# Kernel tuning notes

Hardware: AMD Instinct MI355X
Metric: run time of the kernel (lower is better)

## Reference

```python
import jax, jax.numpy as jnp
import numpy as np

B, N, E, D, DE, H = 2, 50000, 300000, 128, 128, 128
LN_EPS = 1e-5


def setup_inputs() -> dict:
    key = jax.random.key(0)
    ks = jax.random.split(key, 8)
    return {
        "node_features": jax.random.normal(ks[0], (B, N, D), dtype=jnp.float32),
        "edge_features": jax.random.normal(ks[1], (B, E, DE), dtype=jnp.float32),
        "receivers": jax.random.randint(ks[2], (B, E), 0, N, dtype=jnp.int32),
        "W1": jax.random.normal(ks[3], (D + DE, H), dtype=jnp.float32) * (1.0 / np.sqrt(D + DE)),
        "b1": jnp.zeros((H,), dtype=jnp.float32),
        "W2": jax.random.normal(ks[4], (H, D), dtype=jnp.float32) * (1.0 / np.sqrt(H)),
        "b2": jnp.zeros((D,), dtype=jnp.float32),
        "ln_scale": jnp.ones((D,), dtype=jnp.float32),
        "ln_bias": jnp.zeros((D,), dtype=jnp.float32),
    }


def _scatter_mean(edge_features, receivers, n_nodes):
    # batched segment-mean: offset receivers per batch element, one flat segment_sum
    b, e, de = edge_features.shape
    seg = (receivers + jnp.arange(b, dtype=receivers.dtype)[:, None] * n_nodes).reshape(-1)
    sums = jax.ops.segment_sum(edge_features.reshape(b * e, de), seg, num_segments=b * n_nodes)
    cnt = jax.ops.segment_sum(jnp.ones((b * e,), edge_features.dtype), seg, num_segments=b * n_nodes)
    mean = sums / jnp.maximum(cnt, 1.0)[:, None]
    return mean.reshape(b, n_nodes, de)


def reference(node_features, edge_features, receivers, W1, b1, W2, b2, ln_scale, ln_bias):
    n = node_features.shape[1]
    agg = _scatter_mean(edge_features, receivers, n)          # [B, N, DE]
    feat = jnp.concatenate([node_features, agg], axis=-1)     # [B, N, D+DE]
    h = jax.nn.relu(feat @ W1 + b1)                           # [B, N, H]
    out = h @ W2 + b2                                         # [B, N, D]
    mu = jnp.mean(out, axis=-1, keepdims=True)
    var = jnp.mean(jnp.square(out - mu), axis=-1, keepdims=True)
    out = (out - mu) * jax.lax.rsqrt(var + LN_EPS) * ln_scale + ln_bias
    return node_features + out
```

## Files before the change

kernel.cpp:

```cpp
#include <hip/hip_runtime.h>
#include <hip/hip_bf16.h>

#define B_   2
#define N_   50000
#define E_   300000
#define D_   128
#define H_   128
#define K1_  256
#define MTOT (B_ * N_)
#define BM   64
#define CAP  32

typedef __bf16         bf16x8 __attribute__((ext_vector_type(8)));
typedef float          f32x4  __attribute__((ext_vector_type(4)));
typedef unsigned short u16x8  __attribute__((ext_vector_type(8)));
typedef unsigned short u16x4  __attribute__((ext_vector_type(4)));

__device__ __forceinline__ unsigned short f2bf(float f) {
    unsigned u = __builtin_bit_cast(unsigned, f);
    unsigned r = u + 0x7fffu + ((u >> 16) & 1u);
    return (unsigned short)(r >> 16);
}
__device__ __forceinline__ float bf2f(unsigned short h) {
    unsigned u = (unsigned)h << 16;
    return __builtin_bit_cast(float, u);
}

__global__ void wconv_kernel(const float* __restrict__ W1, const float* __restrict__ W2,
                             unsigned short* __restrict__ w1t, unsigned short* __restrict__ w2t,
                             int* __restrict__ deg) {
    int i = blockIdx.x * 256 + threadIdx.x;
    if (i < K1_ * H_) {
        int k = i / H_, n = i % H_;
        w1t[n * K1_ + k] = f2bf(W1[i]);
    }
    if (i < H_ * D_) {
        int k = i / D_, n = i % D_;
        w2t[n * H_ + k] = f2bf(W2[i]);
    }
    for (int j = i; j < MTOT; j += (K1_ * H_)) deg[j] = 0;
}

__global__ __launch_bounds__(256) void fill_kernel(const int* __restrict__ recv,
                                                   int* __restrict__ deg,
                                                   int* __restrict__ eidx) {
    int e = blockIdx.x * 256 + threadIdx.x;
    if (e >= B_ * E_) return;
    int b = e / E_;
    long t = (long)b * N_ + recv[e];
    int slot = atomicAdd(&deg[t], 1);
    if (slot < CAP) eidx[(long)slot * MTOT + t] = e;
}

#define SWZ(byte, row) ((byte) ^ (((row) & 7) << 4))

__global__ __launch_bounds__(256, 4) void fused_kernel(
        const float* __restrict__ nodef, const float* __restrict__ ef,
        const int* __restrict__ deg, const int* __restrict__ eidx,
        const unsigned short* __restrict__ w1t, const unsigned short* __restrict__ w2t,
        const float* __restrict__ b1, const float* __restrict__ b2,
        const float* __restrict__ lnsc, const float* __restrict__ lnbi,
        float* __restrict__ out) {
    __shared__ __align__(16) unsigned short sF[BM * K1_];
    char* sFb = (char*)sF;

    const int tid   = threadIdx.x;
    const long row0 = (long)blockIdx.x * BM;
    const int lane  = tid & 63;
    const int wave  = tid >> 6;

    const int nl = lane >> 2;
    const int ql = lane & 3;
    const int gr = wave * 16 + nl;
    const long ggrow = row0 + gr;
    int dg = 0;
    if (ggrow < MTOT) dg = deg[ggrow];
    int dgc = min(dg, CAP);
    int e0 = (dgc > 0) ? eidx[ggrow] : 0;

    {
        const int seg = tid & 15;
        const int rb  = tid >> 4;
        #pragma unroll
        for (int it = 0; it < 4; ++it) {
            int r = it * 16 + rb;
            long grow = row0 + r;
            u16x8 o;
            if (grow < MTOT) {
                const f32x4* p = (const f32x4*)&nodef[grow * 128 + seg * 8];
                f32x4 x = __builtin_nontemporal_load(p);
                f32x4 y = __builtin_nontemporal_load(p + 1);
                o[0] = f2bf(x[0]); o[1] = f2bf(x[1]);
                o[2] = f2bf(x[2]); o[3] = f2bf(x[3]);
                o[4] = f2bf(y[0]); o[5] = f2bf(y[1]);
                o[6] = f2bf(y[2]); o[7] = f2bf(y[3]);
            } else {
                #pragma unroll
                for (int q = 0; q < 8; ++q) o[q] = 0;
            }
            *(u16x8*)(sFb + SWZ(r * 512 + seg * 16, r)) = o;
        }
    }

    f32x4 ga[8];
    #pragma unroll
    for (int c = 0; c < 8; ++c) { f32x4 z = {0.f, 0.f, 0.f, 0.f}; ga[c] = z; }
    int e = e0;
    for (int i = 0; i < dgc; ++i) {
        int e_next = (i + 1 < dgc) ? eidx[(long)(i + 1) * MTOT + ggrow] : 0;
        const char* base = (const char*)ef + (long)e * 512 + ql * 16;
        #pragma unroll
        for (int c = 0; c < 8; ++c) {
            f32x4 v = __builtin_nontemporal_load((const f32x4*)(base + c * 64));
            ga[c] += v;
        }
        e = e_next;
    }
    {
        float inv = 1.0f / fmaxf((float)dg, 1.0f);
        #pragma unroll
        for (int c = 0; c < 8; ++c) {
            u16x4 o;
            o[0] = f2bf(ga[c][0] * inv); o[1] = f2bf(ga[c][1] * inv);
            o[2] = f2bf(ga[c][2] * inv); o[3] = f2bf(ga[c][3] * inv);
            *(u16x4*)(sFb + SWZ(gr * 512 + 256 + (c * 4 + ql) * 8, gr)) = o;
        }
    }
    __syncthreads();

    const int cl    = lane & 15;
    const int kg    = lane >> 4;
    const int mbase = wave * 16;

    f32x4 acc[8];
    #pragma unroll
    for (int t = 0; t < 8; ++t) { f32x4 z = {0.f, 0.f, 0.f, 0.f}; acc[t] = z; }
    #pragma unroll
    for (int kk = 0; kk < 8; ++kk) {
        bf16x8 a = *(const bf16x8*)(sFb + SWZ(((mbase + cl) << 9) + (kk << 6) + (kg << 4), cl));
        #pragma unroll
        for (int t = 0; t < 8; ++t) {
            bf16x8 b = *(const bf16x8*)&w1t[(t * 16 + cl) * 256 + kk * 32 + kg * 8];
            acc[t] = __builtin_amdgcn_mfma_f32_16x16x32_bf16(a, b, acc[t], 0, 0, 0);
        }
    }
    #pragma unroll
    for (int t = 0; t < 8; ++t) {
        int col = t * 16 + cl;
        float bb = b1[col];
        #pragma unroll
        for (int j = 0; j < 4; ++j) {
            int rl = mbase + kg * 4 + j;
            *(unsigned short*)(sFb + SWZ((rl << 9) + 256 + (col << 1), rl)) =
                f2bf(fmaxf(acc[t][j] + bb, 0.0f));
        }
    }

    f32x4 acc2[8];
    #pragma unroll
    for (int t = 0; t < 8; ++t) { f32x4 z = {0.f, 0.f, 0.f, 0.f}; acc2[t] = z; }
    #pragma unroll
    for (int kk = 0; kk < 4; ++kk) {
        bf16x8 a = *(const bf16x8*)(sFb + SWZ(((mbase + cl) << 9) + 256 + (kk << 6) + (kg << 4), cl));
        #pragma unroll
        for (int t = 0; t < 8; ++t) {
            bf16x8 b = *(const bf16x8*)&w2t[(t * 16 + cl) * 128 + kk * 32 + kg * 8];
            acc2[t] = __builtin_amdgcn_mfma_f32_16x16x32_bf16(a, b, acc2[t], 0, 0, 0);
        }
    }

    float b2v[8], scv[8], biv[8];
    #pragma unroll
    for (int t = 0; t < 8; ++t) {
        int col = t * 16 + cl;
        b2v[t] = b2[col]; scv[t] = lnsc[col]; biv[t] = lnbi[col];
    }
    #pragma unroll
    for (int j = 0; j < 4; ++j) {
        int rl = mbase + kg * 4 + j;
        long grow = row0 + rl;
        float v[8], s = 0.f, s2 = 0.f;
        #pragma unroll
        for (int t = 0; t < 8; ++t) {
            v[t] = acc2[t][j] + b2v[t];
            s += v[t]; s2 += v[t] * v[t];
        }
        #pragma unroll
        for (int m = 1; m < 16; m <<= 1) {
            s  += __shfl_xor(s, m, 16);
            s2 += __shfl_xor(s2, m, 16);
        }
        float mu   = s * (1.0f / 128.0f);
        float var  = s2 * (1.0f / 128.0f) - mu * mu;
        float rstd = rsqrtf(var + 1e-5f);
        if (grow < MTOT) {
            #pragma unroll
            for (int t = 0; t < 8; ++t) {
                int col = t * 16 + cl;
                float nd = bf2f(*(const unsigned short*)(sFb + SWZ((rl << 9) + (col << 1), rl)));
                float res = nd + (v[t] - mu) * rstd * scv[t] + biv[t];
                __builtin_nontemporal_store(res, &out[grow * 128 + col]);
            }
        }
    }
}

extern "C" void kernel_launch(void* const* d_in, const int* in_sizes, int n_in,
                              void* d_out, int out_size, void* d_ws, size_t ws_size,
                              hipStream_t stream) {
    const float* nodef = (const float*)d_in[0];
    const float* ef    = (const float*)d_in[1];
    const int*   recv  = (const int*)d_in[2];
    const float* W1    = (const float*)d_in[3];
    const float* b1    = (const float*)d_in[4];
    const float* W2    = (const float*)d_in[5];
    const float* b2    = (const float*)d_in[6];
    const float* lnsc  = (const float*)d_in[7];
    const float* lnbi  = (const float*)d_in[8];
    float* out = (float*)d_out;

    int* deg  = (int*)d_ws;
    int* eidx = deg + MTOT;
    unsigned short* w1t = (unsigned short*)(eidx + (size_t)MTOT * CAP);
    unsigned short* w2t = w1t + (size_t)H_ * K1_;

    wconv_kernel<<<(K1_ * H_ + 255) / 256, 256, 0, stream>>>(W1, W2, w1t, w2t, deg);

    fill_kernel<<<(B_ * E_ + 255) / 256, 256, 0, stream>>>(recv, deg, eidx);

    fused_kernel<<<(MTOT + BM - 1) / BM, 256, 0, stream>>>(
        nodef, ef, deg, eidx, w1t, w2t, b1, b2, lnsc, lnbi, out);
}
```

Before: 193.3 us.

## Pre-quantize edge features to fp8 and gather compressed rows in fused kernel

The fill kernel now also streams all edge features, converting them to packed fp8 in a workspace buffer. The fused kernel gathers 128-byte fp8 rows per edge instead of 512-byte fp32 rows and decodes them before accumulating. This shrinks random-gather traffic but adds a full sequential read of the edge tensor plus a write and reread of the fp8 copy, and lowers accuracy of the aggregated features.

```diff
diff --git a/kernel.cpp b/kernel.cpp
--- a/kernel.cpp
+++ b/kernel.cpp
@@ -13,8 +13,9 @@
 
 typedef __bf16         bf16x8 __attribute__((ext_vector_type(8)));
 typedef float          f32x4  __attribute__((ext_vector_type(4)));
+typedef float          f32x2  __attribute__((ext_vector_type(2)));
 typedef unsigned short u16x8  __attribute__((ext_vector_type(8)));
-typedef unsigned short u16x4  __attribute__((ext_vector_type(4)));
+typedef unsigned int   u32x4  __attribute__((ext_vector_type(4)));
 
 __device__ __forceinline__ unsigned short f2bf(float f) {
     unsigned u = __builtin_bit_cast(unsigned, f);
@@ -43,19 +44,35 @@
 
 __global__ __launch_bounds__(256) void fill_kernel(const int* __restrict__ recv,
                                                    int* __restrict__ deg,
-                                                   int* __restrict__ eidx) {
-    int e = blockIdx.x * 256 + threadIdx.x;
-    if (e >= B_ * E_) return;
-    int b = e / E_;
-    long t = (long)b * N_ + recv[e];
-    int slot = atomicAdd(&deg[t], 1);
-    if (slot < CAP) eidx[(long)slot * MTOT + t] = e;
+                                                   int* __restrict__ eidx,
+                                                   const float* __restrict__ ef,
+                                                   uint2* __restrict__ efq) {
+    long gid = (long)blockIdx.x * 256 + threadIdx.x;
+    if (gid < (long)B_ * E_) {
+        int e = (int)gid;
+        int b = e / E_;
+        long t = (long)b * N_ + recv[e];
+        int slot = atomicAdd(&deg[t], 1);
+        if (slot < CAP) eidx[(long)slot * MTOT + t] = e;
+    }
+    const long NG  = (long)B_ * E_ * 16;
+    const long GTH = (long)(((long)B_ * E_ + 255) / 256) * 256;
+    for (long g = gid; g < NG; g += GTH) {
+        f32x4 x = __builtin_nontemporal_load((const f32x4*)&ef[g * 8]);
+        f32x4 y = __builtin_nontemporal_load((const f32x4*)&ef[g * 8 + 4]);
+        int lo = __builtin_amdgcn_cvt_pk_fp8_f32(x[0], x[1], 0, 0);
+        lo     = __builtin_amdgcn_cvt_pk_fp8_f32(x[2], x[3], lo, 1);
+        int hi = __builtin_amdgcn_cvt_pk_fp8_f32(y[0], y[1], 0, 0);
+        hi     = __builtin_amdgcn_cvt_pk_fp8_f32(y[2], y[3], hi, 1);
+        uint2 o; o.x = (unsigned)lo; o.y = (unsigned)hi;
+        efq[g] = o;
+    }
 }
 
 #define SWZ(byte, row) ((byte) ^ (((row) & 7) << 4))
 
 __global__ __launch_bounds__(256, 4) void fused_kernel(
-        const float* __restrict__ nodef, const float* __restrict__ ef,
+        const float* __restrict__ nodef, const unsigned int* __restrict__ efq,
         const int* __restrict__ deg, const int* __restrict__ eidx,
         const unsigned short* __restrict__ w1t, const unsigned short* __restrict__ w2t,
         const float* __restrict__ b1, const float* __restrict__ b2,
@@ -108,23 +125,38 @@
     int e = e0;
     for (int i = 0; i < dgc; ++i) {
         int e_next = (i + 1 < dgc) ? eidx[(long)(i + 1) * MTOT + ggrow] : 0;
-        const char* base = (const char*)ef + (long)e * 512 + ql * 16;
-        #pragma unroll
-        for (int c = 0; c < 8; ++c) {
-            f32x4 v = __builtin_nontemporal_load((const f32x4*)(base + c * 64));
-            ga[c] += v;
+        const u32x4* r = (const u32x4*)efq + (long)e * 8;
+        u32x4 A  = r[ql];
+        u32x4 Bv = r[ql + 4];
+        #pragma unroll
+        for (int d = 0; d < 4; ++d) {
+            f32x2 p0 = __builtin_amdgcn_cvt_pk_f32_fp8(A[d], 0);
+            f32x2 p1 = __builtin_amdgcn_cvt_pk_f32_fp8(A[d], 1);
+            ga[d][0] += p0[0]; ga[d][1] += p0[1]; ga[d][2] += p1[0]; ga[d][3] += p1[1];
+        }
+        #pragma unroll
+        for (int d = 0; d < 4; ++d) {
+            f32x2 p0 = __builtin_amdgcn_cvt_pk_f32_fp8(Bv[d], 0);
+            f32x2 p1 = __builtin_amdgcn_cvt_pk_f32_fp8(Bv[d], 1);
+            ga[4 + d][0] += p0[0]; ga[4 + d][1] += p0[1]; ga[4 + d][2] += p1[0]; ga[4 + d][3] += p1[1];
         }
         e = e_next;
     }
     {
         float inv = 1.0f / fmaxf((float)dg, 1.0f);
-        #pragma unroll
-        for (int c = 0; c < 8; ++c) {
-            u16x4 o;
-            o[0] = f2bf(ga[c][0] * inv); o[1] = f2bf(ga[c][1] * inv);
-            o[2] = f2bf(ga[c][2] * inv); o[3] = f2bf(ga[c][3] * inv);
-            *(u16x4*)(sFb + SWZ(gr * 512 + 256 + (c * 4 + ql) * 8, gr)) = o;
-        }
+        u16x8 o;
+        #pragma unroll
+        for (int j = 0; j < 4; ++j) { o[j] = f2bf(ga[0][j] * inv); o[4 + j] = f2bf(ga[1][j] * inv); }
+        *(u16x8*)(sFb + SWZ(gr * 512 + 256 + 32 * ql, gr)) = o;
+        #pragma unroll
+        for (int j = 0; j < 4; ++j) { o[j] = f2bf(ga[2][j] * inv); o[4 + j] = f2bf(ga[3][j] * inv); }
+        *(u16x8*)(sFb + SWZ(gr * 512 + 256 + 32 * ql + 16, gr)) = o;
+        #pragma unroll
+        for (int j = 0; j < 4; ++j) { o[j] = f2bf(ga[4][j] * inv); o[4 + j] = f2bf(ga[5][j] * inv); }
+        *(u16x8*)(sFb + SWZ(gr * 512 + 384 + 32 * ql, gr)) = o;
+        #pragma unroll
+        for (int j = 0; j < 4; ++j) { o[j] = f2bf(ga[6][j] * inv); o[4 + j] = f2bf(ga[7][j] * inv); }
+        *(u16x8*)(sFb + SWZ(gr * 512 + 384 + 32 * ql + 16, gr)) = o;
     }
     __syncthreads();
 
@@ -219,15 +251,16 @@
     const float* lnbi  = (const float*)d_in[8];
     float* out = (float*)d_out;
 
-    int* deg  = (int*)d_ws;
+    uint2* efq = (uint2*)d_ws;
+    int* deg  = (int*)((char*)d_ws + (size_t)B_ * E_ * 128);
     int* eidx = deg + MTOT;
     unsigned short* w1t = (unsigned short*)(eidx + (size_t)MTOT * CAP);
     unsigned short* w2t = w1t + (size_t)H_ * K1_;
 
     wconv_kernel<<<(K1_ * H_ + 255) / 256, 256, 0, stream>>>(W1, W2, w1t, w2t, deg);
 
-    fill_kernel<<<(B_ * E_ + 255) / 256, 256, 0, stream>>>(recv, deg, eidx);
+    fill_kernel<<<(B_ * E_ + 255) / 256, 256, 0, stream>>>(recv, deg, eidx, ef, efq);
 
     fused_kernel<<<(MTOT + BM - 1) / BM, 256, 0, stream>>>(
-        nodef, ef, deg, eidx, w1t, w2t, b1, b2, lnsc, lnbi, out);
-}
+        nodef, (const unsigned int*)efq, deg, eidx, w1t, w2t, b1, b2, lnsc, lnbi, out);
+}
```

New measurement: 221.6 us. +14.6%, slower.
